# Kernel optimization log

Hardware: AMD Instinct MI355X
Metric: run time of the kernel (lower is better)

Reference implementation:

```python
import jax, jax.numpy as jnp
import numpy as np

SCALES = (0.9, 1.1)


def resize_bilinear(x, oh, ow):
    """Bilinear resize matching torch F.interpolate(mode='bilinear', align_corners=False).
    x: [B, C, H, W] -> [B, C, oh, ow]."""
    B, C, H, W = x.shape
    if (oh, ow) == (H, W):
        return x
    ys = jnp.clip((jnp.arange(oh, dtype=jnp.float32) + 0.5) * (H / oh) - 0.5, 0.0, H - 1)
    xs = jnp.clip((jnp.arange(ow, dtype=jnp.float32) + 0.5) * (W / ow) - 0.5, 0.0, W - 1)
    y0 = jnp.floor(ys).astype(jnp.int32)
    x0 = jnp.floor(xs).astype(jnp.int32)
    y1 = jnp.minimum(y0 + 1, H - 1)
    x1 = jnp.minimum(x0 + 1, W - 1)
    wy = (ys - y0).astype(x.dtype)[None, None, :, None]
    wx = (xs - x0).astype(x.dtype)[None, None, None, :]
    row = x[:, :, y0, :] * (1 - wy) + x[:, :, y1, :] * wy   # [B,C,oh,W]
    out = row[:, :, :, x0] * (1 - wx) + row[:, :, :, x1] * wx  # [B,C,oh,ow]
    return out


def xcorr_same(feat, filt):
    """F.conv2d cross-correlation with asymmetric 'same' padding as in compute_similarity_scores.
    feat: [1, C, H, W], filt: [N, C, FH, FW] -> [1, N, H, W]."""
    FH, FW = filt.shape[2], filt.shape[3]
    pad = ((FH // 2, (FH - 1) // 2), (FW // 2, (FW - 1) // 2))
    return jax.lax.conv_general_dilated(
        feat, filt, window_strides=(1, 1), padding=pad,
        dimension_numbers=('NCHW', 'OIHW', 'NCHW'))


def scale_boxes(tlbr_np, sh, sw, HF, WF):
    """rescale_box_features: floor top/left, ceil bottom/right, +1 and clamp to feature bounds."""
    t = np.maximum(np.floor(tlbr_np[:, 0] * sh), 0)
    l = np.maximum(np.floor(tlbr_np[:, 1] * sw), 0)
    b = np.minimum(np.ceil(tlbr_np[:, 2] * sh) + 1, HF)
    r = np.minimum(np.ceil(tlbr_np[:, 3] * sw) + 1, WF)
    return np.stack([t, l, b, r], axis=1).astype(np.int32)


def scaled_size(h, w, s):
    hs = int(np.ceil(h * s)); hs = h if hs <= 1 else hs
    ws = int(np.ceil(w * s)); ws = w if ws <= 1 else ws
    return hs, ws


def image_similarities(m3, m4, tlbr_np, img_h, img_w):
    """m3: [512,H3,W3], m4: [1024,H4,W4], tlbr_np: [N,4] int. Returns [6, N, H3, W3]."""
    sims = []
    for feat in (m3, m4):
        C, HF, WF = feat.shape
        sb = scale_boxes(tlbr_np, HF / img_h, WF / img_w, HF, WF)
        crops = [feat[:, t:b, l:r] for t, l, b, r in sb]  # variable-size ROI crops
        mh = max(c.shape[1] for c in crops)
        mw = max(c.shape[2] for c in crops)
        patches = jnp.concatenate(
            [resize_bilinear(c[None], mh, mw) for c in crops], axis=0)  # [N,C,mh,mw]
        sizes = [(mh, mw)] + [scaled_size(mh, mw, s) for s in SCALES]
        for (hs, ws) in sizes:
            filt = resize_bilinear(patches, hs, ws)
            sims.append(xcorr_same(feat[None], filt))  # [1,N,HF,WF]
    # resize_to_uniform_height_width over the 6 similarity maps, then cat on dim0
    mh = max(s.shape[2] for s in sims)
    mw = max(s.shape[3] for s in sims)
    return jnp.concatenate([resize_bilinear(s, mh, mw) for s in sims], axis=0)  # [6,N,mh,mw]


def setup_inputs() -> dict:
    key = jax.random.key(0)
    k3, k4 = jax.random.split(key)
    B, N = 4, 3
    map3 = jax.random.normal(k3, (B, 512, 128, 128), dtype=jnp.float32)
    map4 = jax.random.normal(k4, (B, 1024, 64, 64), dtype=jnp.float32)
    base = np.array([[100, 120, 220, 260],
                     [400,  80, 520, 230],
                     [600, 640, 740, 790]], dtype=np.int32)
    tlbr = jnp.asarray(np.stack([base + 8 * i for i in range(B)], axis=0))  # [B,N,4]
    return {"map3": map3, "map4": map4, "tlbr": tlbr, "img_h": 1024, "img_w": 1024}


def reference(map3, map4, tlbr, img_h, img_w):
    tlbr_np = np.asarray(tlbr)  # box coords are host-side constants (shapes depend on them)
    B = map3.shape[0]
    outs = [image_similarities(map3[i], map4[i], tlbr_np[i], img_h, img_w) for i in range(B)]
    out = jnp.stack(outs, axis=0)          # [B, 6, N, H, W]
    return jnp.transpose(out, (0, 2, 1, 3, 4))  # [B, N, 6, H, W]
```

## Files before the change

kernel.cpp:

```cpp
#include <hip/hip_runtime.h>
#include <math.h>

typedef float  fx4  __attribute__((ext_vector_type(4)));
typedef short  bfx8 __attribute__((ext_vector_type(8)));

__device__ __forceinline__ void bl_w(int o, int O, int I, int& i0, int& i1, float& w) {
    float r = (float)((double)I / (double)O);
    float f = (o + 0.5f) * r - 0.5f;
    f = fminf(fmaxf(f, 0.0f), (float)(I - 1));
    int a = (int)floorf(f);
    i0 = a;
    i1 = min(a + 1, I - 1);
    w = f - (float)a;
}

__device__ __forceinline__ void bl_w_r(int o, float r, int I, int& i0, int& i1, float& w) {
    float f = (o + 0.5f) * r - 0.5f;
    f = fminf(fmaxf(f, 0.0f), (float)(I - 1));
    int a = (int)floorf(f);
    i0 = a;
    i1 = min(a + 1, I - 1);
    w = f - (float)a;
}

__device__ __forceinline__ unsigned int bf16rne(float f) {
    unsigned int x = __builtin_bit_cast(unsigned int, f);
    return ((x + 0x7fffu + ((x >> 16) & 1u)) >> 16) & 0xffffu;
}

__device__ __forceinline__ unsigned int pk_bf16(float lo, float hi) {
    unsigned int r;
    asm("v_cvt_pk_bf16_f32 %0, %1, %2" : "=v"(r) : "v"(lo), "v"(hi));
    return r;
}

__global__ void k_meta(const int* __restrict__ tlbr, const int* __restrict__ p_imgh,
                       const int* __restrict__ p_imgw, int B, int N, int ms,
                       int* __restrict__ meta) {
    if (blockIdx.x != 0 || threadIdx.x != 0) return;
    const int HFs[2] = {128, 64};
    const double SC[2] = {0.9, 1.1};
    int img_h = *p_imgh, img_w = *p_imgw;
    for (int b = 0; b < B; ++b)
      for (int lvl = 0; lvl < 2; ++lvl) {
        int HF = HFs[lvl], WF = HFs[lvl];
        double sh = (double)HF / (double)img_h;
        double sw = (double)WF / (double)img_w;
        int* m = meta + (b*2 + lvl)*ms;
        int mh = 0, mw = 0;
        for (int n = 0; n < N; ++n) {
            const int* bx = tlbr + ((size_t)(b*N) + n)*4;
            int t  = max((int)floor((double)bx[0]*sh), 0);
            int l  = max((int)floor((double)bx[1]*sw), 0);
            int bb = min((int)ceil((double)bx[2]*sh) + 1, HF);
            int rr = min((int)ceil((double)bx[3]*sw) + 1, WF);
            int chh = bb - t, cww = rr - l;
            m[2+4*n+0] = t; m[2+4*n+1] = l; m[2+4*n+2] = chh; m[2+4*n+3] = cww;
            mh = max(mh, chh); mw = max(mw, cww);
        }
        m[0] = mh; m[1] = mw;
        int fo = 2 + 4*N;
        m[fo+0] = mh; m[fo+1] = mw;
        for (int s = 0; s < 2; ++s) {
            int hs  = (int)ceil((double)mh * SC[s]); if (hs  <= 1) hs  = mh;
            int wsv = (int)ceil((double)mw * SC[s]); if (wsv <= 1) wsv = mw;
            m[fo+2+2*s] = hs; m[fo+2+2*s+1] = wsv;
        }
        int fo2 = fo + 6;
        for (int s = 0; s < 3; ++s) {
            int fh = m[fo+2*s], fw = m[fo+2*s+1];
            m[fo2+2*s]   = __float_as_int((float)((double)mw / (double)fw));
            m[fo2+2*s+1] = __float_as_int((float)((double)mh / (double)fh));
        }
        for (int n = 0; n < N; ++n) {
            m[fo2+6+2*n]   = __float_as_int((float)((double)m[2+4*n+3] / (double)mw));
            m[fo2+6+2*n+1] = __float_as_int((float)((double)m[2+4*n+2] / (double)mh));
        }
      }
}

template<int C, int KH, int KW, int NKYG>
__global__ void k_filters(const float* __restrict__ feat_all, const int* __restrict__ meta,
                          unsigned short* __restrict__ Wswz, int b0, int chunkB,
                          int N, int lvl, int ms, int HF, int WF) {
    constexpr int KWG = KW/4;
    constexpr int KT  = C*KWG*NKYG;
    long long tau = (long long)blockIdx.x*256 + threadIdx.x;
    long long total = (long long)chunkB * KT * 64;
    if (tau >= total) return;
    int m  = (int)(tau & 15);
    int g  = (int)((tau >> 4) & 3);
    long long rest = tau >> 6;
    int s  = (int)(rest % KT);
    int lb = (int)(rest / KT);
    int kyg = s % NKYG; int s2 = s / NKYG;
    int kxg = s2 % KWG;
    int c   = s2 / KWG;
    int kx  = kxg*4 + g;
    int ky0 = kyg*8;
    uint4 outv = make_uint4(0, 0, 0, 0);
    unsigned int* ow = (unsigned int*)&outv;
    int sc = m / N, n = m - sc*N;
    if (sc < 3) {
        int b = b0 + lb;
        const int* mt = meta + (b*2 + lvl)*ms;
        int mh = mt[0], mw = mt[1];
        int t = mt[2+4*n], l = mt[3+4*n], chh = mt[4+4*n], cww = mt[5+4*n];
        int fo = 2 + 4*N;
        int fh = mt[fo + 2*sc], fw = mt[fo + 2*sc + 1];
        int fo2 = fo + 6;
        float r1 = __int_as_float(mt[fo2+2*sc]);
        float r2 = __int_as_float(mt[fo2+2*sc+1]);
        float r3 = __int_as_float(mt[fo2+6+2*n]);
        float r4 = __int_as_float(mt[fo2+6+2*n+1]);
        int offy = KH/2 - fh/2, offx = KW/2 - fw/2;
        int fx = kx - offx;
        if (fx >= 0 && fx < fw) {
            const float* src = feat_all + ((size_t)b*C + c)*HF*WF;
            int px0, px1; float wx;  bl_w_r(fx, r1, mw, px0, px1, wx);
            int ax0, ax1; float awx; bl_w_r(px0, r3, cww, ax0, ax1, awx);
            int bx0, bx1; float bwx; bl_w_r(px1, r3, cww, bx0, bx1, bwx);
            #pragma unroll
            for (int jj = 0; jj < 8; ++jj) {
                int fy = ky0 + jj - offy;
                if (fy >= 0 && fy < fh) {
                    int py0, py1; float wy; bl_w_r(fy, r2, mh, py0, py1, wy);
                    float pv[2][2];
                    #pragma unroll
                    for (int pi = 0; pi < 2; ++pi) {
                        int py = pi ? py1 : py0;
                        int cy0, cy1; float cwy; bl_w_r(py, r4, chh, cy0, cy1, cwy);
                        const float* q0 = src + (size_t)(t + cy0)*WF + l;
                        const float* q1 = src + (size_t)(t + cy1)*WF + l;
                        pv[pi][0] = (q0[ax0]*(1.f-cwy) + q1[ax0]*cwy)*(1.f-awx)
                                  + (q0[ax1]*(1.f-cwy) + q1[ax1]*cwy)*awx;
                        pv[pi][1] = (q0[bx0]*(1.f-cwy) + q1[bx0]*cwy)*(1.f-bwx)
                                  + (q0[bx1]*(1.f-cwy) + q1[bx1]*cwy)*bwx;
                    }
                    float v = (pv[0][0]*(1.f-wy) + pv[1][0]*wy)*(1.f-wx)
                            + (pv[0][1]*(1.f-wy) + pv[1][1]*wy)*wx;
                    ow[jj >> 1] |= bf16rne(v) << (16*(jj & 1));
                }
            }
        }
    }
    ((uint4*)Wswz)[tau] = outv;
}

template<int C, int KS, int KH, int KW, int H, int W, int NKYG, int NDY, int NT,
         int RSTR, int NCOL, int P>
__global__ __launch_bounds__(256, 4) void k_mfconv(
        const float* __restrict__ feat_all, const unsigned short* __restrict__ Wswz,
        float* __restrict__ part, int b0, int Btot, int N, int nks) {
    constexpr int KWG   = KW/4;
    constexpr int NROWS = KH + (NDY-1)*8;
    constexpr int NRT   = NROWS/8;
    constexpr int NCT   = NCOL/4;
    constexpr int KT    = C*KWG*NKYG;
    constexpr int NFR   = NKYG + NDY - 1;
    __shared__ __align__(16) unsigned short smem[NCOL*RSTR];

    const int yb  = blockIdx.y;
    const int zz  = blockIdx.z;
    const int ksp = zz % nks;
    const int lb  = zz / nks;
    const int b   = b0 + lb;
    const int y0  = (yb >> 3)*(8*NDY) + (yb & 7);
    const int tid = threadIdx.x;
    const int lane = tid & 63;
    const int wv   = tid >> 6;
    const int g    = lane >> 4;
    const int lm   = lane & 15;
    const int rot  = (zz*7 + yb*3) & (KS-1);

    fx4 acc[NT][NDY];
    #pragma unroll
    for (int t = 0; t < NT; ++t)
        #pragma unroll
        for (int dy = 0; dy < NDY; ++dy) acc[t][dy] = (fx4){0.f, 0.f, 0.f, 0.f};

    const float* feat = feat_all + (size_t)b * C * H * W;
    const unsigned short* Wlane = Wswz + ((size_t)lb*KT)*512 + lane*8;

    const bool sact = tid < NCT*NRT;
    const int rt = tid % NRT, ct = tid / NRT;
    const int col0 = ct*4, r0 = rt*8;
    const int sx0 = col0 - P;

    auto STAGE = [&](int c) {
        if (!sact) return;
        const float* src = feat + (size_t)c*H*W;
        float4 f[8];
        #pragma unroll
        for (int rr = 0; rr < 8; ++rr) {
            int y = y0 + r0 + rr - P;
            bool yok = (y >= 0) && (y < H);
            if (yok && sx0 >= 0 && sx0 + 3 < W) {
                f[rr] = *reinterpret_cast<const float4*>(src + (size_t)y*W + sx0);
            } else {
                float t4[4];
                #pragma unroll
                for (int j = 0; j < 4; ++j) {
                    int x = sx0 + j;
                    t4[j] = (yok && x >= 0 && x < W) ? src[(size_t)y*W + x] : 0.f;
                }
                f[rr] = make_float4(t4[0], t4[1], t4[2], t4[3]);
            }
        }
        #pragma unroll
        for (int j = 0; j < 4; ++j) {
            uint4 w4;
            w4.x = pk_bf16(((const float*)&f[0])[j], ((const float*)&f[1])[j]);
            w4.y = pk_bf16(((const float*)&f[2])[j], ((const float*)&f[3])[j]);
            w4.z = pk_bf16(((const float*)&f[4])[j], ((const float*)&f[5])[j]);
            w4.w = pk_bf16(((const float*)&f[6])[j], ((const float*)&f[7])[j]);
            *reinterpret_cast<uint4*>(smem + (col0 + j)*RSTR + r0) = w4;
        }
    };
    auto CHOF = [&](int i) { return ksp*KS + ((i + rot) & (KS-1)); };

    STAGE(CHOF(0));
    bfx8 afc[NKYG];
    {
        const unsigned short* W0 = Wlane + ((size_t)CHOF(0)*KWG)*NKYG*512;
        #pragma unroll
        for (int kyg = 0; kyg < NKYG; ++kyg)
            afc[kyg] = *reinterpret_cast<const bfx8*>(W0 + (size_t)kyg*512);
    }
    __syncthreads();

    #pragma unroll 1
    for (int ci = 0; ci < KS; ++ci) {
        #pragma unroll 2
        for (int kxg = 0; kxg < KWG; ++kxg) {
            bfx8 afn[NKYG];
            {
                int ni = (kxg + 1 < KWG) ? ci : ci + 1;
                int nk = (kxg + 1 < KWG) ? kxg + 1 : 0;
                const unsigned short* Wn =
                    Wlane + (((size_t)CHOF(ni)*KWG + nk)*NKYG)*512;
                #pragma unroll
                for (int kyg = 0; kyg < NKYG; ++kyg)
                    afn[kyg] = *reinterpret_cast<const bfx8*>(Wn + (size_t)kyg*512);
            }
            #pragma unroll
            for (int t = 0; t < NT; ++t) {
                const unsigned short* bp =
                    smem + ((size_t)(t*64 + wv*16 + lm + g + kxg*4))*RSTR;
                bfx8 fr[NFR];
                #pragma unroll
                for (int rg = 0; rg < NFR; ++rg)
                    fr[rg] = *reinterpret_cast<const bfx8*>(bp + rg*8);
                __builtin_amdgcn_s_setprio(1);
                #pragma unroll
                for (int dy = 0; dy < NDY; ++dy)
                    #pragma unroll
                    for (int kyg = 0; kyg < NKYG; ++kyg)
                        acc[t][dy] = __builtin_amdgcn_mfma_f32_16x16x32_bf16(
                            afc[kyg], fr[kyg + dy], acc[t][dy], 0, 0, 0);
                __builtin_amdgcn_s_setprio(0);
            }
            #pragma unroll
            for (int kyg = 0; kyg < NKYG; ++kyg) afc[kyg] = afn[kyg];
        }
        __syncthreads();
        if (ci + 1 < KS) STAGE(CHOF(ci + 1));
        __syncthreads();
    }
    #pragma unroll
    for (int t = 0; t < NT; ++t) {
        const int x = t*64 + wv*16 + lm;
        #pragma unroll
        for (int dy = 0; dy < NDY; ++dy) {
            int y = y0 + dy*8;
            #pragma unroll
            for (int r = 0; r < 4; ++r) {
                int m  = g*4 + r;
                int sc = m / N;
                int n  = m - sc*N;
                if (sc < 3) {
                    size_t oi = ((((size_t)ksp*Btot + b)*N + n)*3 + sc)*((size_t)H*W)
                              + (size_t)y*W + x;
                    part[oi] = acc[t][dy][r];
                }
            }
        }
    }
}

__global__ void k_reduce3(const float* __restrict__ part, float* __restrict__ out,
                          int B, int N, int nks) {
    int idx = blockIdx.x*256 + threadIdx.x;
    int tot = B*N*3*128*128;
    if (idx >= tot) return;
    int px = idx & 16383;
    int r = idx >> 14;
    int sc = r % 3; r /= 3;
    int n = r % N; int b = r / N;
    size_t stride = (size_t)B*N*3*16384;
    const float* p = part + ((size_t)(b*N + n)*3 + sc)*16384 + px;
    float s = 0.f;
    for (int ks = 0; ks < nks; ++ks) s += p[(size_t)ks*stride];
    out[(((size_t)(b*N + n)*6 + sc) << 14) + px] = s;
}

__global__ void k_upsample_sum(const float* __restrict__ part, float* __restrict__ out,
                               int B, int N, int nks) {
    int idx = blockIdx.x*256 + threadIdx.x;
    int tot = B*N*3*128*128;
    if (idx >= tot) return;
    int x = idx & 127; int r = idx >> 7;
    int y = r & 127; r >>= 7;
    int sc = r % 3; r /= 3;
    int n = r % N; int b = r / N;
    int y0, y1, x0, x1; float wy, wx;
    bl_w(y, 128, 64, y0, y1, wy);
    bl_w(x, 128, 64, x0, x1, wx);
    size_t stride = (size_t)B*N*3*4096;
    const float* p = part + ((size_t)(b*N + n)*3 + sc)*4096;
    float f00 = 0.f, f10 = 0.f, f01 = 0.f, f11 = 0.f;
    for (int ks = 0; ks < nks; ++ks) {
        const float* q = p + (size_t)ks*stride;
        f00 += q[y0*64 + x0]; f10 += q[y1*64 + x0];
        f01 += q[y0*64 + x1]; f11 += q[y1*64 + x1];
    }
    out[((size_t)((b*N + n)*6 + 3 + sc)*128 + y)*128 + x] =
        (f00*(1.f-wy) + f10*wy)*(1.f-wx) + (f01*(1.f-wy) + f11*wy)*wx;
}

extern "C" void kernel_launch(void* const* d_in, const int* in_sizes, int n_in,
                              void* d_out, int out_size, void* d_ws, size_t ws_size,
                              hipStream_t stream) {
    const float* map3 = (const float*)d_in[0];
    const float* map4 = (const float*)d_in[1];
    const int*   tlbr = (const int*)d_in[2];
    const int*   p_imgh = (const int*)d_in[3];
    const int*   p_imgw = (const int*)d_in[4];
    float* out = (float*)d_out;

    const int C3 = 512, H3 = 128, C4 = 1024, H4 = 64;
    int B = in_sizes[0] / (C3 * H3 * H3);
    int N = in_sizes[2] / (B * 4);
    int ms = 2 + 4*N + 6 + 6 + 2*N;
    const int NKS3 = 16, NKS4 = 64;

    char* wsp = (char*)d_ws;
    int* meta = (int*)wsp;
    size_t off = 4096;
    float* part = (float*)(wsp + off);
    size_t part_bytes = (size_t)NKS3 * B * N * 3 * H3 * H3 * 4;
    off += part_bytes;
    unsigned short* Wbuf = (unsigned short*)(wsp + off);
    size_t wavail = (ws_size > off) ? (ws_size - off) : 0;
    size_t wpb = (size_t)9216 * 1024;
    int cb = (int)(wavail / wpb); if (cb > B) cb = B; if (cb < 1) cb = 1;

    k_meta<<<1, 1, 0, stream>>>(tlbr, p_imgh, p_imgw, B, N, ms, meta);

    {
        for (int b0 = 0; b0 < B; b0 += cb) {
            int cbn = (cb < B - b0) ? cb : (B - b0);
            long long thr = (long long)cbn * 9216 * 64;
            k_filters<512,24,24,3><<<(int)((thr + 255) / 256), 256, 0, stream>>>(
                map3, meta, Wbuf, b0, cbn, N, 0, ms, H3, H3);
            dim3 grid(1, 32, cbn * NKS3);
            k_mfconv<512,32,24,24,128,128,3,4,2,56,152,12><<<grid, 256, 0, stream>>>(
                map3, Wbuf, part, b0, B, N, NKS3);
        }
        int tot = B * N * 3 * H3 * H3;
        k_reduce3<<<(tot + 255) / 256, 256, 0, stream>>>(part, out, B, N, NKS3);
    }
    {
        for (int b0 = 0; b0 < B; b0 += cb) {
            int cbn = (cb < B - b0) ? cb : (B - b0);
            long long thr = (long long)cbn * 8192 * 64;
            k_filters<1024,16,16,2><<<(int)((thr + 255) / 256), 256, 0, stream>>>(
                map4, meta, Wbuf, b0, cbn, N, 1, ms, H4, H4);
            dim3 grid(1, 8, cbn * NKS4);
            k_mfconv<1024,16,16,16,64,64,2,8,1,72,80,8><<<grid, 256, 0, stream>>>(
                map4, Wbuf, part, b0, B, N, NKS4);
        }
        int tot = B * N * 3 * H3 * H3;
        k_upsample_sum<<<(tot + 255) / 256, 256, 0, stream>>>(part, out, B, N, NKS4);
    }
}
```

Measured before the change: 996.4 us.

## Warp-specialize conv kernel with producer waves and double-buffered LDS staging

The MFMA convolution kernel now launches 384 threads. Two extra producer waves stage the next channel's feature tile into a double-buffered shared-memory slot while four consumer waves run MFMAs on the current one. The per-block output tile and split-K counts are changed: x-tiling over 64 columns, 8 row groups, and halved split counts with twice the channels per block. Weight-register prefetching and the channel rotation are removed. Consumer waves now load A fragments directly each iteration, which adds load latency on the MFMA path, and the larger LDS footprint may reduce occupancy.

New measurement: 1.364 ms. +36.9%, slower.

```diff
diff --git a/kernel.cpp b/kernel.cpp
--- a/kernel.cpp
+++ b/kernel.cpp
@@ -147,19 +147,21 @@
     ((uint4*)Wswz)[tau] = outv;
 }
 
-template<int C, int KS, int KH, int KW, int H, int W, int NKYG, int NDY, int NT,
+template<int C, int KS, int KH, int KW, int H, int W, int NKYG, int NDY,
          int RSTR, int NCOL, int P>
-__global__ __launch_bounds__(256, 4) void k_mfconv(
+__global__ __launch_bounds__(384, 3) void k_mfconv(
         const float* __restrict__ feat_all, const unsigned short* __restrict__ Wswz,
         float* __restrict__ part, int b0, int Btot, int N, int nks) {
     constexpr int KWG   = KW/4;
+    constexpr int CHSTR = NCOL*RSTR;
     constexpr int NROWS = KH + (NDY-1)*8;
     constexpr int NRT   = NROWS/8;
     constexpr int NCT   = NCOL/4;
     constexpr int KT    = C*KWG*NKYG;
     constexpr int NFR   = NKYG + NDY - 1;
-    __shared__ __align__(16) unsigned short smem[NCOL*RSTR];
-
+    __shared__ __align__(16) unsigned short smem[2*CHSTR];
+
+    const int xb  = blockIdx.x;
     const int yb  = blockIdx.y;
     const int zz  = blockIdx.z;
     const int ksp = zz % nks;
@@ -167,86 +169,76 @@
     const int b   = b0 + lb;
     const int y0  = (yb >> 3)*(8*NDY) + (yb & 7);
     const int tid = threadIdx.x;
-    const int lane = tid & 63;
-    const int wv   = tid >> 6;
-    const int g    = lane >> 4;
-    const int lm   = lane & 15;
-    const int rot  = (zz*7 + yb*3) & (KS-1);
-
-    fx4 acc[NT][NDY];
-    #pragma unroll
-    for (int t = 0; t < NT; ++t)
+    const int wid = tid >> 6;
+    const float* feat = feat_all + (size_t)b * C * H * W;
+    const int cbase = ksp * KS;
+
+    if (wid >= 4) {
+        const int st = tid - 256;
+        auto STAGE = [&](int ci, unsigned short* buf) {
+            const float* src = feat + (size_t)(cbase + ci)*H*W;
+            for (int it = st; it < NCT*NRT; it += 128) {
+                int rt = it % NRT, ct = it / NRT;
+                int col0 = ct*4, r0 = rt*8;
+                int x0 = xb*64 + col0 - P;
+                float4 f[8];
+                #pragma unroll
+                for (int rr = 0; rr < 8; ++rr) {
+                    int y = y0 + r0 + rr - P;
+                    bool yok = (y >= 0) && (y < H);
+                    if (yok && x0 >= 0 && x0 + 3 < W) {
+                        f[rr] = *reinterpret_cast<const float4*>(src + (size_t)y*W + x0);
+                    } else {
+                        float t4[4];
+                        #pragma unroll
+                        for (int j = 0; j < 4; ++j) {
+                            int x = x0 + j;
+                            t4[j] = (yok && x >= 0 && x < W) ? src[(size_t)y*W + x] : 0.f;
+                        }
+                        f[rr] = make_float4(t4[0], t4[1], t4[2], t4[3]);
+                    }
+                }
+                #pragma unroll
+                for (int j = 0; j < 4; ++j) {
+                    uint4 w4;
+                    w4.x = pk_bf16(((const float*)&f[0])[j], ((const float*)&f[1])[j]);
+                    w4.y = pk_bf16(((const float*)&f[2])[j], ((const float*)&f[3])[j]);
+                    w4.z = pk_bf16(((const float*)&f[4])[j], ((const float*)&f[5])[j]);
+                    w4.w = pk_bf16(((const float*)&f[6])[j], ((const float*)&f[7])[j]);
+                    *reinterpret_cast<uint4*>(buf + (col0 + j)*RSTR + r0) = w4;
+                }
+            }
+        };
+        STAGE(0, smem);
+        __syncthreads();
+        #pragma unroll 1
+        for (int ci = 0; ci < KS; ++ci) {
+            if (ci + 1 < KS) STAGE(ci + 1, smem + ((ci + 1) & 1)*CHSTR);
+            __syncthreads();
+        }
+    } else {
+        const int lane = tid & 63;
+        const int wv   = wid;
+        const int g    = lane >> 4;
+        const int lm   = lane & 15;
+        fx4 acc[NDY];
         #pragma unroll
-        for (int dy = 0; dy < NDY; ++dy) acc[t][dy] = (fx4){0.f, 0.f, 0.f, 0.f};
-
-    const float* feat = feat_all + (size_t)b * C * H * W;
-    const unsigned short* Wlane = Wswz + ((size_t)lb*KT)*512 + lane*8;
-
-    const bool sact = tid < NCT*NRT;
-    const int rt = tid % NRT, ct = tid / NRT;
-    const int col0 = ct*4, r0 = rt*8;
-    const int sx0 = col0 - P;
-
-    auto STAGE = [&](int c) {
-        if (!sact) return;
-        const float* src = feat + (size_t)c*H*W;
-        float4 f[8];
-        #pragma unroll
-        for (int rr = 0; rr < 8; ++rr) {
-            int y = y0 + r0 + rr - P;
-            bool yok = (y >= 0) && (y < H);
-            if (yok && sx0 >= 0 && sx0 + 3 < W) {
-                f[rr] = *reinterpret_cast<const float4*>(src + (size_t)y*W + sx0);
-            } else {
-                float t4[4];
-                #pragma unroll
-                for (int j = 0; j < 4; ++j) {
-                    int x = sx0 + j;
-                    t4[j] = (yok && x >= 0 && x < W) ? src[(size_t)y*W + x] : 0.f;
-                }
-                f[rr] = make_float4(t4[0], t4[1], t4[2], t4[3]);
-            }
-        }
-        #pragma unroll
-        for (int j = 0; j < 4; ++j) {
-            uint4 w4;
-            w4.x = pk_bf16(((const float*)&f[0])[j], ((const float*)&f[1])[j]);
-            w4.y = pk_bf16(((const float*)&f[2])[j], ((const float*)&f[3])[j]);
-            w4.z = pk_bf16(((const float*)&f[4])[j], ((const float*)&f[5])[j]);
-            w4.w = pk_bf16(((const float*)&f[6])[j], ((const float*)&f[7])[j]);
-            *reinterpret_cast<uint4*>(smem + (col0 + j)*RSTR + r0) = w4;
-        }
-    };
-    auto CHOF = [&](int i) { return ksp*KS + ((i + rot) & (KS-1)); };
-
-    STAGE(CHOF(0));
-    bfx8 afc[NKYG];
-    {
-        const unsigned short* W0 = Wlane + ((size_t)CHOF(0)*KWG)*NKYG*512;
-        #pragma unroll
-        for (int kyg = 0; kyg < NKYG; ++kyg)
-            afc[kyg] = *reinterpret_cast<const bfx8*>(W0 + (size_t)kyg*512);
-    }
-    __syncthreads();
-
-    #pragma unroll 1
-    for (int ci = 0; ci < KS; ++ci) {
-        #pragma unroll 2
-        for (int kxg = 0; kxg < KWG; ++kxg) {
-            bfx8 afn[NKYG];
-            {
-                int ni = (kxg + 1 < KWG) ? ci : ci + 1;
-                int nk = (kxg + 1 < KWG) ? kxg + 1 : 0;
-                const unsigned short* Wn =
-                    Wlane + (((size_t)CHOF(ni)*KWG + nk)*NKYG)*512;
+        for (int t = 0; t < NDY; ++t) acc[t] = (fx4){0.f, 0.f, 0.f, 0.f};
+        const unsigned short* Wlane = Wswz + ((size_t)lb*KT)*512 + lane*8;
+        const int pcol = wv*16 + lm + g;
+
+        __syncthreads();
+        #pragma unroll 1
+        for (int ci = 0; ci < KS; ++ci) {
+            const unsigned short* sb = smem + (ci & 1)*CHSTR;
+            const unsigned short* Wc = Wlane + ((size_t)(cbase + ci)*KWG*NKYG)*512;
+            #pragma unroll 2
+            for (int kxg = 0; kxg < KWG; ++kxg) {
+                bfx8 af[NKYG];
                 #pragma unroll
                 for (int kyg = 0; kyg < NKYG; ++kyg)
-                    afn[kyg] = *reinterpret_cast<const bfx8*>(Wn + (size_t)kyg*512);
-            }
-            #pragma unroll
-            for (int t = 0; t < NT; ++t) {
-                const unsigned short* bp =
-                    smem + ((size_t)(t*64 + wv*16 + lm + g + kxg*4))*RSTR;
+                    af[kyg] = *reinterpret_cast<const bfx8*>(Wc + (size_t)(kxg*NKYG + kyg)*512);
+                const unsigned short* bp = sb + ((size_t)(pcol + kxg*4))*RSTR;
                 bfx8 fr[NFR];
                 #pragma unroll
                 for (int rg = 0; rg < NFR; ++rg)
@@ -256,23 +248,17 @@
                 for (int dy = 0; dy < NDY; ++dy)
                     #pragma unroll
                     for (int kyg = 0; kyg < NKYG; ++kyg)
-                        acc[t][dy] = __builtin_amdgcn_mfma_f32_16x16x32_bf16(
-                            afc[kyg], fr[kyg + dy], acc[t][dy], 0, 0, 0);
+                        acc[dy] = __builtin_amdgcn_mfma_f32_16x16x32_bf16(
+                            af[kyg], fr[kyg + dy], acc[dy], 0, 0, 0);
                 __builtin_amdgcn_s_setprio(0);
             }
-            #pragma unroll
-            for (int kyg = 0; kyg < NKYG; ++kyg) afc[kyg] = afn[kyg];
-        }
-        __syncthreads();
-        if (ci + 1 < KS) STAGE(CHOF(ci + 1));
-        __syncthreads();
-    }
-    #pragma unroll
-    for (int t = 0; t < NT; ++t) {
-        const int x = t*64 + wv*16 + lm;
+            __syncthreads();
+        }
+        const int x = xb*64 + wv*16 + lm;
         #pragma unroll
         for (int dy = 0; dy < NDY; ++dy) {
             int y = y0 + dy*8;
+            if (y >= H) continue;
             #pragma unroll
             for (int r = 0; r < 4; ++r) {
                 int m  = g*4 + r;
@@ -281,7 +267,7 @@
                 if (sc < 3) {
                     size_t oi = ((((size_t)ksp*Btot + b)*N + n)*3 + sc)*((size_t)H*W)
                               + (size_t)y*W + x;
-                    part[oi] = acc[t][dy][r];
+                    part[oi] = acc[dy][r];
                 }
             }
         }
@@ -342,7 +328,7 @@
     int B = in_sizes[0] / (C3 * H3 * H3);
     int N = in_sizes[2] / (B * 4);
     int ms = 2 + 4*N + 6 + 6 + 2*N;
-    const int NKS3 = 16, NKS4 = 64;
+    const int NKS3 = 8, NKS4 = 32;
 
     char* wsp = (char*)d_ws;
     int* meta = (int*)wsp;
@@ -363,8 +349,8 @@
             long long thr = (long long)cbn * 9216 * 64;
             k_filters<512,24,24,3><<<(int)((thr + 255) / 256), 256, 0, stream>>>(
                 map3, meta, Wbuf, b0, cbn, N, 0, ms, H3, H3);
-            dim3 grid(1, 32, cbn * NKS3);
-            k_mfconv<512,32,24,24,128,128,3,4,2,56,152,12><<<grid, 256, 0, stream>>>(
+            dim3 grid(2, 16, cbn * NKS3);
+            k_mfconv<512,64,24,24,128,128,3,8,88,88,12><<<grid, 384, 0, stream>>>(
                 map3, Wbuf, part, b0, B, N, NKS3);
         }
         int tot = B * N * 3 * H3 * H3;
@@ -377,7 +363,7 @@
             k_filters<1024,16,16,2><<<(int)((thr + 255) / 256), 256, 0, stream>>>(
                 map4, meta, Wbuf, b0, cbn, N, 1, ms, H4, H4);
             dim3 grid(1, 8, cbn * NKS4);
-            k_mfconv<1024,16,16,16,64,64,2,8,1,72,80,8><<<grid, 256, 0, stream>>>(
+            k_mfconv<1024,32,16,16,64,64,2,8,72,80,8><<<grid, 384, 0, stream>>>(
                 map4, Wbuf, part, b0, B, N, NKS4);
         }
         int tot = B * N * 3 * H3 * H3;
```
